# Kernel optimization log

Measured on AMD Instinct MI355X. Metric: run time of the kernel, lower is better.

Reference implementation:

```python
import math
import jax, jax.numpy as jnp
import numpy as np

E = 1024
H = 16
HD = E // H
MLP = 4 * E
EPS = 1e-6


def setup_inputs() -> dict:
    key = jax.random.key(0)
    ks = jax.random.split(key, 12)
    s = lambda fan_in: 1.0 / math.sqrt(fan_in)
    return {
        "x": jax.random.normal(ks[0], (8, 1024, E), dtype=jnp.float32),
        "ln1_g": jnp.ones((E,), jnp.float32),
        "ln1_b": jnp.zeros((E,), jnp.float32),
        "w_qkv": jax.random.normal(ks[1], (E, 3 * E), jnp.float32) * s(E),
        "b_qkv": jnp.zeros((3 * E,), jnp.float32),
        "w_o": jax.random.normal(ks[2], (E, E), jnp.float32) * s(E),
        "b_o": jnp.zeros((E,), jnp.float32),
        "ln2_g": jnp.ones((E,), jnp.float32),
        "ln2_b": jnp.zeros((E,), jnp.float32),
        "w_fc1": jax.random.normal(ks[3], (E, MLP), jnp.float32) * s(E),
        "b_fc1": jnp.zeros((MLP,), jnp.float32),
        "w_fc2": jax.random.normal(ks[4], (MLP, E), jnp.float32) * s(MLP),
        "b_fc2": jnp.zeros((E,), jnp.float32),
    }


def _layernorm(x, g, b):
    mu = jnp.mean(x, axis=-1, keepdims=True)
    var = jnp.mean(jnp.square(x - mu), axis=-1, keepdims=True)
    return (x - mu) * jax.lax.rsqrt(var + EPS) * g + b


def _attn(x, w_qkv, b_qkv, w_o, b_o):
    B, N, _ = x.shape
    qkv = (x @ w_qkv + b_qkv).reshape(B, N, 3, H, HD)
    q, k, v = qkv[:, :, 0], qkv[:, :, 1], qkv[:, :, 2]  # [B,N,H,HD]
    scores = jnp.einsum("bnhd,bmhd->bhnm", q, k) / math.sqrt(HD)
    probs = jax.nn.softmax(scores, axis=-1)
    out = jnp.einsum("bhnm,bmhd->bnhd", probs, v).reshape(B, N, H * HD)
    return out @ w_o + b_o


def reference(x, ln1_g, ln1_b, w_qkv, b_qkv, w_o, b_o, ln2_g, ln2_b,
              w_fc1, b_fc1, w_fc2, b_fc2):
    # pre-LN attention block with residual
    x = x + _attn(_layernorm(x, ln1_g, ln1_b), w_qkv, b_qkv, w_o, b_o)
    # pre-LN MLP block with residual (exact GELU, matching torch nn.GELU)
    h = _layernorm(x, ln2_g, ln2_b) @ w_fc1 + b_fc1
    h = jax.nn.gelu(h, approximate=False)
    x = x + (h @ w_fc2 + b_fc2)
    return x
```

## Files before the change

kernel.cpp:

```cpp
#include <hip/hip_runtime.h>
#include <stdint.h>

typedef unsigned short u16;
typedef __bf16 bf16x8 __attribute__((ext_vector_type(8)));
typedef float f32x4 __attribute__((ext_vector_type(4)));

#define GLD16(gp, lp) __builtin_amdgcn_global_load_lds( \
    (__attribute__((address_space(1))) void*)(uintptr_t)(gp), \
    (__attribute__((address_space(3))) void*)(uintptr_t)(lp), 16, 0, 0)

#define WAITVM(N) asm volatile("s_waitcnt vmcnt(" #N ")" ::: "memory")
#define BARRIER() asm volatile("s_barrier" ::: "memory")
#define MM(a, b, c) __builtin_amdgcn_mfma_f32_16x16x32_bf16(a, b, c, 0, 0, 0)

__device__ __forceinline__ u16 f2bf(float f) {
  uint32_t u = __builtin_bit_cast(uint32_t, f);
  u += 0x7FFFu + ((u >> 16) & 1u);
  return (u16)(u >> 16);
}

__global__ __launch_bounds__(256) void wtrans(const float* __restrict__ w,
                                              u16* __restrict__ wt, int K, int Nn) {
  __shared__ float tile[64][68];
  const int c0 = blockIdx.x << 6, r0 = blockIdx.y << 6;
  const int t = threadIdx.x, tr = t >> 2, tc = t & 3;
#pragma unroll
  for (int p = 0; p < 4; ++p) {
    float4 v = *(const float4*)&w[(size_t)(r0 + tr) * Nn + c0 + tc * 4 + p * 16];
    tile[tr][tc * 4 + p * 16 + 0] = v.x;
    tile[tr][tc * 4 + p * 16 + 1] = v.y;
    tile[tr][tc * 4 + p * 16 + 2] = v.z;
    tile[tr][tc * 4 + p * 16 + 3] = v.w;
  }
  __syncthreads();
#pragma unroll
  for (int p = 0; p < 4; ++p) {
    u16 e0 = f2bf(tile[tc * 4 + p * 16 + 0][tr]);
    u16 e1 = f2bf(tile[tc * 4 + p * 16 + 1][tr]);
    u16 e2 = f2bf(tile[tc * 4 + p * 16 + 2][tr]);
    u16 e3 = f2bf(tile[tc * 4 + p * 16 + 3][tr]);
    uint2 o;
    o.x = (uint32_t)e0 | ((uint32_t)e1 << 16);
    o.y = (uint32_t)e2 | ((uint32_t)e3 << 16);
    *(uint2*)&wt[(size_t)(c0 + tr) * K + r0 + tc * 4 + p * 16] = o;
  }
}

__global__ __launch_bounds__(256) void lnorm(const float* x, const float* __restrict__ g,
                                             const float* __restrict__ bta,
                                             u16* __restrict__ out) {
  const int lane = threadIdx.x & 63, wid = threadIdx.x >> 6;
  const size_t token = (size_t)blockIdx.x * 4 + wid;
  const float* row = x + token * 1024;
  float v[16];
#pragma unroll
  for (int i = 0; i < 4; ++i) {
    float4 f = *(const float4*)&row[(lane + i * 64) * 4];
    v[i * 4 + 0] = f.x; v[i * 4 + 1] = f.y; v[i * 4 + 2] = f.z; v[i * 4 + 3] = f.w;
  }
  float s = 0.f, s2 = 0.f;
#pragma unroll
  for (int i = 0; i < 16; ++i) { s += v[i]; s2 += v[i] * v[i]; }
  for (int off = 1; off < 64; off <<= 1) {
    s += __shfl_xor(s, off);
    s2 += __shfl_xor(s2, off);
  }
  const float mu = s * (1.0f / 1024.0f);
  const float var = s2 * (1.0f / 1024.0f) - mu * mu;
  const float rstd = rsqrtf(var + 1e-6f);
  u16* orow = out + token * 1024;
#pragma unroll
  for (int i = 0; i < 4; ++i) {
    const int c = (lane + i * 64) * 4;
    float4 gv = *(const float4*)&g[c];
    float4 bv = *(const float4*)&bta[c];
    u16 e0 = f2bf((v[i * 4 + 0] - mu) * rstd * gv.x + bv.x);
    u16 e1 = f2bf((v[i * 4 + 1] - mu) * rstd * gv.y + bv.y);
    u16 e2 = f2bf((v[i * 4 + 2] - mu) * rstd * gv.z + bv.z);
    u16 e3 = f2bf((v[i * 4 + 3] - mu) * rstd * gv.w + bv.w);
    uint2 o;
    o.x = (uint32_t)e0 | ((uint32_t)e1 << 16);
    o.y = (uint32_t)e2 | ((uint32_t)e3 << 16);
    *(uint2*)&orow[c] = o;
  }
}

template <int EPI>
__global__ __launch_bounds__(512, 2) void gemmk(const u16* __restrict__ A,
                                                const u16* __restrict__ Bt,
                                                const float* __restrict__ bias,
                                                void* Cout, int Ndim, int K, int nT,
                                                float qscale, int qlimit, int gn) {
  __shared__ __align__(16) u16 lds[4][16384];
  const int tid = threadIdx.x, lane = tid & 63, wid = tid >> 6;
  const int wm = wid >> 2, wn = wid & 3;

  const int wg = blockIdx.x;
  const int swz = (wg & 7) * ((int)gridDim.x >> 3) + (wg >> 3);
  const int mblk = swz / gn, nb = swz - mblk * gn;
  const int m0 = mblk << 8, n0 = nb << 8;
  const int koff = blockIdx.y * (nT << 5);

  const int srow = tid >> 2;
  const int gsub = (tid & 3) ^ ((tid >> 3) & 3);
  const u16* Ag = A + koff + (size_t)(m0 + srow) * K + gsub * 8;
  const u16* Bg = Bt + koff + (size_t)(n0 + srow) * K + gsub * 8;
  const size_t rstep = (size_t)128 * K;
  char* lb = (char*)&lds[0][0];

  const int rrow = lane & 15, g = lane >> 4;
  const int xg = g ^ ((rrow >> 1) & 3);
  const int aoff = (wm * 128 + rrow) * 64 + xg * 16;
  const int boff = 16384 + (wn * 64 + rrow) * 64 + xg * 16;

  const f32x4 fzero = {0.f, 0.f, 0.f, 0.f};
  f32x4 acc[8][4];
#pragma unroll
  for (int i = 0; i < 8; ++i)
#pragma unroll
    for (int j = 0; j < 4; ++j) acc[i][j] = fzero;

#define STG(tt) do { \
    char* d_ = lb + ((tt) & 3) * 32768; \
    GLD16(Ag + (size_t)(tt) * 32, d_ + tid * 16); \
    GLD16(Ag + rstep + (size_t)(tt) * 32, d_ + 8192 + tid * 16); \
    GLD16(Bg + (size_t)(tt) * 32, d_ + 16384 + tid * 16); \
    GLD16(Bg + rstep + (size_t)(tt) * 32, d_ + 24576 + tid * 16); \
  } while (0)

  STG(0);
  STG(1);
  WAITVM(4);
  BARRIER();
  for (int t = 0; t < nT; ++t) {
    if (t + 2 < nT) STG(t + 2);
    const char* sb = lb + (t & 3) * 32768;
    bf16x8 bfr[4], af[8];
#pragma unroll
    for (int nf = 0; nf < 4; ++nf)
      bfr[nf] = *(const bf16x8*)(sb + boff + nf * 1024);
#pragma unroll
    for (int mf = 0; mf < 8; ++mf)
      af[mf] = *(const bf16x8*)(sb + aoff + mf * 1024);
    __builtin_amdgcn_s_setprio(1);
#pragma unroll
    for (int mf = 0; mf < 8; ++mf)
#pragma unroll
      for (int nf = 0; nf < 4; ++nf)
        acc[mf][nf] = MM(af[mf], bfr[nf], acc[mf][nf]);
    __builtin_amdgcn_s_setprio(0);
    if (t + 1 < nT) {
      if (t < nT - 2) { WAITVM(4); } else { WAITVM(0); }
      BARRIER();
    }
  }
#undef STG

  const int g4 = (lane >> 4) << 2;
#pragma unroll
  for (int nf = 0; nf < 4; ++nf) {
    const int col = n0 + wn * 64 + nf * 16 + rrow;
    const float bvb = (EPI == 3 && blockIdx.y != 0) ? 0.0f : bias[col];
    const float csf = (EPI == 0 && col < qlimit) ? qscale : 1.0f;
#pragma unroll
    for (int mf = 0; mf < 8; ++mf) {
#pragma unroll
      for (int r = 0; r < 4; ++r) {
        const int row = m0 + wm * 128 + mf * 16 + g4 + r;
        float v = acc[mf][nf][r] + bvb;
        if (EPI == 0) v *= csf;
        if (EPI == 1) v = 0.5f * v * (1.0f + erff(v * 0.70710678118654752f));
        if (EPI == 3) {
          atomicAdd((float*)Cout + (size_t)row * Ndim + col, v);
        } else {
          ((u16*)Cout)[(size_t)row * Ndim + col] = f2bf(v);
        }
      }
    }
  }
}

__global__ __launch_bounds__(256) void vtrans(const u16* __restrict__ qkv,
                                              u16* __restrict__ vt) {
  const int bh = blockIdx.y, b = bh >> 4, h = bh & 15;
  const int n0 = blockIdx.x << 6;
  __shared__ __align__(16) u16 tile[64][72];
  const int t = threadIdx.x, r = t >> 2, c = t & 3;
  const u16* src = qkv + (size_t)((b << 10) + n0 + r) * 3072 + 2048 + (h << 6);
#pragma unroll
  for (int p = 0; p < 2; ++p)
    *(uint4*)&tile[r][(c * 2 + p) * 8] = *(const uint4*)(src + (c * 2 + p) * 8);
  __syncthreads();
  u16* dst = vt + (size_t)((bh << 6) + r) * 1024 + n0;
#pragma unroll
  for (int p = 0; p < 2; ++p) {
    u16 o[8];
#pragma unroll
    for (int j = 0; j < 8; ++j) o[j] = tile[(c * 2 + p) * 8 + j][r];
    uint4 w;
    w.x = (uint32_t)o[0] | ((uint32_t)o[1] << 16);
    w.y = (uint32_t)o[2] | ((uint32_t)o[3] << 16);
    w.z = (uint32_t)o[4] | ((uint32_t)o[5] << 16);
    w.w = (uint32_t)o[6] | ((uint32_t)o[7] << 16);
    *(uint4*)&dst[(c * 2 + p) * 8] = w;
  }
}

__global__ __launch_bounds__(256) void attn64(const u16* __restrict__ qkv,
                                              const u16* __restrict__ vt,
                                              u16* __restrict__ aout) {
  const int bh = blockIdx.y, b = bh >> 4, h = bh & 15;
  const int q0 = blockIdx.x << 6;
  const int tid = threadIdx.x, lane = tid & 63, wid = tid >> 6;
  __shared__ __align__(16) u16 kl[4096];
  __shared__ __align__(16) u16 vl[4096];
  __shared__ __align__(16) u16 pl[4][1152];

  const int rrow = lane & 15;
  const int g = lane >> 4;
  const u16* qrow = qkv + (size_t)((b << 10) + q0 + (wid << 4) + rrow) * 3072 + (h << 6);
  bf16x8 qf0 = *(const bf16x8*)(qrow + (g << 3));
  bf16x8 qf1 = *(const bf16x8*)(qrow + 32 + (g << 3));

  const int sr = lane >> 3;
  const int lc = (lane & 7) ^ sr;
  const u16* kbase = qkv + (size_t)(b << 10) * 3072 + 1024 + (h << 6) +
                     (size_t)(16 * wid + sr) * 3072 + lc * 8;
  const u16* vbase = vt + (size_t)(bh << 6) * 1024 + (size_t)(16 * wid + sr) * 1024 + lc * 8;

  const f32x4 fzero = {0.f, 0.f, 0.f, 0.f};
  f32x4 oacc[4];
#pragma unroll
  for (int i = 0; i < 4; ++i) oacc[i] = fzero;
  f32x4 lacc = fzero;
  const int rcb = lane & 7;
  u16* plw = &pl[wid][0];

  for (int t = 0; t < 16; ++t) {
    const int kt0 = t << 6;
    GLD16(kbase + (size_t)kt0 * 3072, &kl[(2 * wid + 0) * 512]);
    GLD16(kbase + (size_t)kt0 * 3072 + 8 * 3072, &kl[(2 * wid + 1) * 512]);
    GLD16(vbase + kt0, &vl[(2 * wid + 0) * 512]);
    GLD16(vbase + kt0 + 8 * 1024, &vl[(2 * wid + 1) * 512]);
    __syncthreads();

    f32x4 s4[4];
#pragma unroll
    for (int i = 0; i < 4; ++i) s4[i] = fzero;
#pragma unroll
    for (int nf = 0; nf < 4; ++nf) {
      bf16x8 k0 = *(const bf16x8*)((const char*)kl + (nf * 16 + rrow) * 128 +
                                   ((g + 0) ^ rcb) * 16);
      bf16x8 k1 = *(const bf16x8*)((const char*)kl + (nf * 16 + rrow) * 128 +
                                   ((g + 4) ^ rcb) * 16);
      s4[nf] = __builtin_amdgcn_mfma_f32_16x16x32_bf16(k0, qf0, s4[nf], 0, 0, 0);
      s4[nf] = __builtin_amdgcn_mfma_f32_16x16x32_bf16(k1, qf1, s4[nf], 0, 0, 0);
    }

#pragma unroll
    for (int nf = 0; nf < 4; ++nf) {
      float p0 = exp2f(s4[nf][0]);
      float p1 = exp2f(s4[nf][1]);
      float p2 = exp2f(s4[nf][2]);
      float p3 = exp2f(s4[nf][3]);
      f32x4 pv = {p0, p1, p2, p3};
      lacc += pv;
      uint32_t a0 = __builtin_bit_cast(uint32_t, p0) + 0x8000u;
      uint32_t a1 = __builtin_bit_cast(uint32_t, p1) + 0x8000u;
      uint32_t a2 = __builtin_bit_cast(uint32_t, p2) + 0x8000u;
      uint32_t a3 = __builtin_bit_cast(uint32_t, p3) + 0x8000u;
      uint2 w;
      w.x = __builtin_amdgcn_perm(a1, a0, 0x07060302);
      w.y = __builtin_amdgcn_perm(a3, a2, 0x07060302);
      *(uint2*)(plw + rrow * 72 + nf * 16 + (g << 2)) = w;
    }

    bf16x8 pf0 = *(const bf16x8*)((const char*)plw + rrow * 144 + (g << 4));
    bf16x8 pf1 = *(const bf16x8*)((const char*)plw + rrow * 144 + (g << 4) + 64);
#pragma unroll
    for (int nf = 0; nf < 4; ++nf) {
      bf16x8 v0 = *(const bf16x8*)((const char*)vl + (nf * 16 + rrow) * 128 +
                                   ((g + 0) ^ rcb) * 16);
      bf16x8 v1 = *(const bf16x8*)((const char*)vl + (nf * 16 + rrow) * 128 +
                                   ((g + 4) ^ rcb) * 16);
      oacc[nf] = __builtin_amdgcn_mfma_f32_16x16x32_bf16(pf0, v0, oacc[nf], 0, 0, 0);
      oacc[nf] = __builtin_amdgcn_mfma_f32_16x16x32_bf16(pf1, v1, oacc[nf], 0, 0, 0);
    }
    __syncthreads();
  }

  float lsum = lacc[0] + lacc[1] + lacc[2] + lacc[3];
  lsum += __shfl_xor(lsum, 16);
  lsum += __shfl_xor(lsum, 32);
  const float inv = 1.0f / lsum;
  float invq[4];
#pragma unroll
  for (int r = 0; r < 4; ++r) {
    int bi = __builtin_amdgcn_ds_bpermute(((g << 2) + r) << 2,
                                          __builtin_bit_cast(int, inv));
    invq[r] = __builtin_bit_cast(float, bi);
  }
  u16* ob = aout + (size_t)((b << 10) + q0 + (wid << 4)) * 1024 + (h << 6);
#pragma unroll
  for (int nf = 0; nf < 4; ++nf)
#pragma unroll
    for (int r = 0; r < 4; ++r)
      ob[(size_t)(g * 4 + r) * 1024 + nf * 16 + rrow] = f2bf(oacc[nf][r] * invq[r]);
}

extern "C" void kernel_launch(void* const* d_in, const int* in_sizes, int n_in,
                              void* d_out, int out_size, void* d_ws, size_t ws_size,
                              hipStream_t stream) {
  const float* x = (const float*)d_in[0];
  const float* ln1_g = (const float*)d_in[1];
  const float* ln1_b = (const float*)d_in[2];
  const float* w_qkv = (const float*)d_in[3];
  const float* b_qkv = (const float*)d_in[4];
  const float* w_o = (const float*)d_in[5];
  const float* b_o = (const float*)d_in[6];
  const float* ln2_g = (const float*)d_in[7];
  const float* ln2_b = (const float*)d_in[8];
  const float* w_fc1 = (const float*)d_in[9];
  const float* b_fc1 = (const float*)d_in[10];
  const float* w_fc2 = (const float*)d_in[11];
  const float* b_fc2 = (const float*)d_in[12];
  float* out = (float*)d_out;

  char* w = (char*)d_ws;
  u16* wqkvT = (u16*)w; w += (size_t)3072 * 1024 * 2;
  u16* woT   = (u16*)w; w += (size_t)1024 * 1024 * 2;
  u16* wfc1T = (u16*)w; w += (size_t)4096 * 1024 * 2;
  u16* wfc2T = (u16*)w; w += (size_t)1024 * 4096 * 2;
  u16* xn    = (u16*)w; w += (size_t)8192 * 1024 * 2;
  u16* qkvb  = (u16*)w; w += (size_t)8192 * 3072 * 2;
  u16* vtb   = (u16*)w; w += (size_t)128 * 64 * 1024 * 2;
  u16* attnb = (u16*)w; w += (size_t)8192 * 1024 * 2;
  u16* hbuf  = qkvb;

  const float QS = 0.18033688011112042f;

  wtrans<<<dim3(48, 16), 256, 0, stream>>>(w_qkv, wqkvT, 1024, 3072);
  wtrans<<<dim3(16, 16), 256, 0, stream>>>(w_o, woT, 1024, 1024);
  wtrans<<<dim3(64, 16), 256, 0, stream>>>(w_fc1, wfc1T, 1024, 4096);
  wtrans<<<dim3(16, 64), 256, 0, stream>>>(w_fc2, wfc2T, 4096, 1024);

  lnorm<<<2048, 256, 0, stream>>>(x, ln1_g, ln1_b, xn);
  gemmk<0><<<dim3(384, 1), 512, 0, stream>>>(xn, wqkvT, b_qkv, qkvb, 3072, 1024, 32, QS, 1024, 12);
  vtrans<<<dim3(16, 128), 256, 0, stream>>>(qkvb, vtb);
  attn64<<<dim3(16, 128), 256, 0, stream>>>(qkvb, vtb, attnb);
  hipMemcpyAsync(out, x, (size_t)8192 * 1024 * 4, hipMemcpyDeviceToDevice, stream);
  gemmk<3><<<dim3(128, 2), 512, 0, stream>>>(attnb, woT, b_o, out, 1024, 1024, 16, 1.f, 0, 4);
  lnorm<<<2048, 256, 0, stream>>>(out, ln2_g, ln2_b, xn);
  gemmk<1><<<dim3(512, 1), 512, 0, stream>>>(xn, wfc1T, b_fc1, hbuf, 4096, 1024, 32, 1.f, 0, 16);
  gemmk<3><<<dim3(128, 2), 512, 0, stream>>>(hbuf, wfc2T, b_fc2, out, 1024, 4096, 64, 1.f, 0, 4);
}
```

Baseline: 480.5 us.

## Deepen GEMM pipeline to three stages, split staging, replace split-K atomics with residual epilogue

```diff
diff --git a/kernel.cpp b/kernel.cpp
--- a/kernel.cpp
+++ b/kernel.cpp
@@ -86,11 +86,12 @@
 }
 
 template <int EPI>
-__global__ __launch_bounds__(512, 2) void gemmk(const u16* __restrict__ A,
+__global__ __launch_bounds__(512, 2) void gemmf(const u16* __restrict__ A,
                                                 const u16* __restrict__ Bt,
                                                 const float* __restrict__ bias,
-                                                void* Cout, int Ndim, int K, int nT,
-                                                float qscale, int qlimit, int gn) {
+                                                const float* res, void* Cout,
+                                                int Ndim, int K, float qscale,
+                                                int qlimit, int gn) {
   __shared__ __align__(16) u16 lds[4][16384];
   const int tid = threadIdx.x, lane = tid & 63, wid = tid >> 6;
   const int wm = wid >> 2, wn = wid & 3;
@@ -99,12 +100,11 @@
   const int swz = (wg & 7) * ((int)gridDim.x >> 3) + (wg >> 3);
   const int mblk = swz / gn, nb = swz - mblk * gn;
   const int m0 = mblk << 8, n0 = nb << 8;
-  const int koff = blockIdx.y * (nT << 5);
 
   const int srow = tid >> 2;
   const int gsub = (tid & 3) ^ ((tid >> 3) & 3);
-  const u16* Ag = A + koff + (size_t)(m0 + srow) * K + gsub * 8;
-  const u16* Bg = Bt + koff + (size_t)(n0 + srow) * K + gsub * 8;
+  const u16* Ag = A + (size_t)(m0 + srow) * K + gsub * 8;
+  const u16* Bg = Bt + (size_t)(n0 + srow) * K + gsub * 8;
   const size_t rstep = (size_t)128 * K;
   char* lb = (char*)&lds[0][0];
 
@@ -120,47 +120,69 @@
 #pragma unroll
     for (int j = 0; j < 4; ++j) acc[i][j] = fzero;
 
-#define STG(tt) do { \
-    char* d_ = lb + ((tt) & 3) * 32768; \
+#define STGA(tt) do { char* d_ = lb + ((tt) & 3) * 32768; \
     GLD16(Ag + (size_t)(tt) * 32, d_ + tid * 16); \
-    GLD16(Ag + rstep + (size_t)(tt) * 32, d_ + 8192 + tid * 16); \
+    GLD16(Ag + rstep + (size_t)(tt) * 32, d_ + 8192 + tid * 16); } while (0)
+#define STGB(tt) do { char* d_ = lb + ((tt) & 3) * 32768; \
     GLD16(Bg + (size_t)(tt) * 32, d_ + 16384 + tid * 16); \
-    GLD16(Bg + rstep + (size_t)(tt) * 32, d_ + 24576 + tid * 16); \
-  } while (0)
-
-  STG(0);
-  STG(1);
-  WAITVM(4);
-  BARRIER();
-  for (int t = 0; t < nT; ++t) {
-    if (t + 2 < nT) STG(t + 2);
-    const char* sb = lb + (t & 3) * 32768;
-    bf16x8 bfr[4], af[8];
-#pragma unroll
-    for (int nf = 0; nf < 4; ++nf)
-      bfr[nf] = *(const bf16x8*)(sb + boff + nf * 1024);
-#pragma unroll
-    for (int mf = 0; mf < 8; ++mf)
-      af[mf] = *(const bf16x8*)(sb + aoff + mf * 1024);
+    GLD16(Bg + rstep + (size_t)(tt) * 32, d_ + 24576 + tid * 16); } while (0)
+
+  const int nT = K >> 5;
+  STGA(0); STGB(0);
+  STGA(1); STGB(1);
+  STGA(2); STGB(2);
+
+  for (int k = 0; k < nT; ++k) {
+    if (k < nT - 2) { WAITVM(8); }
+    else if (k == nT - 2) { WAITVM(4); }
+    else { WAITVM(0); }
+    BARRIER();
+    const char* sb = lb + (k & 3) * 32768;
+    const bool st = (k + 3 < nT);
+    if (st) STGA(k + 3);
+    bf16x8 a0 = *(const bf16x8*)(sb + aoff + 0 * 1024);
+    bf16x8 a1 = *(const bf16x8*)(sb + aoff + 1 * 1024);
+    bf16x8 a2 = *(const bf16x8*)(sb + aoff + 2 * 1024);
+    bf16x8 a3 = *(const bf16x8*)(sb + aoff + 3 * 1024);
+    bf16x8 a4 = *(const bf16x8*)(sb + aoff + 4 * 1024);
+    bf16x8 a5 = *(const bf16x8*)(sb + aoff + 5 * 1024);
+    bf16x8 a6 = *(const bf16x8*)(sb + aoff + 6 * 1024);
+    bf16x8 a7 = *(const bf16x8*)(sb + aoff + 7 * 1024);
+    bf16x8 b0 = *(const bf16x8*)(sb + boff + 0 * 1024);
+    bf16x8 b1 = *(const bf16x8*)(sb + boff + 1 * 1024);
     __builtin_amdgcn_s_setprio(1);
-#pragma unroll
-    for (int mf = 0; mf < 8; ++mf)
-#pragma unroll
-      for (int nf = 0; nf < 4; ++nf)
-        acc[mf][nf] = MM(af[mf], bfr[nf], acc[mf][nf]);
+    acc[0][0] = MM(a0, b0, acc[0][0]); acc[1][0] = MM(a1, b0, acc[1][0]);
+    acc[2][0] = MM(a2, b0, acc[2][0]); acc[3][0] = MM(a3, b0, acc[3][0]);
+    acc[4][0] = MM(a4, b0, acc[4][0]); acc[5][0] = MM(a5, b0, acc[5][0]);
+    acc[6][0] = MM(a6, b0, acc[6][0]); acc[7][0] = MM(a7, b0, acc[7][0]);
+    acc[0][1] = MM(a0, b1, acc[0][1]); acc[1][1] = MM(a1, b1, acc[1][1]);
+    acc[2][1] = MM(a2, b1, acc[2][1]); acc[3][1] = MM(a3, b1, acc[3][1]);
+    acc[4][1] = MM(a4, b1, acc[4][1]); acc[5][1] = MM(a5, b1, acc[5][1]);
+    acc[6][1] = MM(a6, b1, acc[6][1]); acc[7][1] = MM(a7, b1, acc[7][1]);
     __builtin_amdgcn_s_setprio(0);
-    if (t + 1 < nT) {
-      if (t < nT - 2) { WAITVM(4); } else { WAITVM(0); }
-      BARRIER();
-    }
-  }
-#undef STG
+    BARRIER();
+    if (st) STGB(k + 3);
+    bf16x8 b2 = *(const bf16x8*)(sb + boff + 2 * 1024);
+    bf16x8 b3 = *(const bf16x8*)(sb + boff + 3 * 1024);
+    __builtin_amdgcn_s_setprio(1);
+    acc[0][2] = MM(a0, b2, acc[0][2]); acc[1][2] = MM(a1, b2, acc[1][2]);
+    acc[2][2] = MM(a2, b2, acc[2][2]); acc[3][2] = MM(a3, b2, acc[3][2]);
+    acc[4][2] = MM(a4, b2, acc[4][2]); acc[5][2] = MM(a5, b2, acc[5][2]);
+    acc[6][2] = MM(a6, b2, acc[6][2]); acc[7][2] = MM(a7, b2, acc[7][2]);
+    acc[0][3] = MM(a0, b3, acc[0][3]); acc[1][3] = MM(a1, b3, acc[1][3]);
+    acc[2][3] = MM(a2, b3, acc[2][3]); acc[3][3] = MM(a3, b3, acc[3][3]);
+    acc[4][3] = MM(a4, b3, acc[4][3]); acc[5][3] = MM(a5, b3, acc[5][3]);
+    acc[6][3] = MM(a6, b3, acc[6][3]); acc[7][3] = MM(a7, b3, acc[7][3]);
+    __builtin_amdgcn_s_setprio(0);
+  }
+#undef STGA
+#undef STGB
 
   const int g4 = (lane >> 4) << 2;
 #pragma unroll
   for (int nf = 0; nf < 4; ++nf) {
     const int col = n0 + wn * 64 + nf * 16 + rrow;
-    const float bvb = (EPI == 3 && blockIdx.y != 0) ? 0.0f : bias[col];
+    const float bvb = bias[col];
     const float csf = (EPI == 0 && col < qlimit) ? qscale : 1.0f;
 #pragma unroll
     for (int mf = 0; mf < 8; ++mf) {
@@ -170,8 +192,9 @@
         float v = acc[mf][nf][r] + bvb;
         if (EPI == 0) v *= csf;
         if (EPI == 1) v = 0.5f * v * (1.0f + erff(v * 0.70710678118654752f));
-        if (EPI == 3) {
-          atomicAdd((float*)Cout + (size_t)row * Ndim + col, v);
+        if (EPI == 2) {
+          v += res[(size_t)row * Ndim + col];
+          ((float*)Cout)[(size_t)row * Ndim + col] = v;
         } else {
           ((u16*)Cout)[(size_t)row * Ndim + col] = f2bf(v);
         }
@@ -345,12 +368,11 @@
   wtrans<<<dim3(16, 64), 256, 0, stream>>>(w_fc2, wfc2T, 4096, 1024);
 
   lnorm<<<2048, 256, 0, stream>>>(x, ln1_g, ln1_b, xn);
-  gemmk<0><<<dim3(384, 1), 512, 0, stream>>>(xn, wqkvT, b_qkv, qkvb, 3072, 1024, 32, QS, 1024, 12);
+  gemmf<0><<<384, 512, 0, stream>>>(xn, wqkvT, b_qkv, nullptr, qkvb, 3072, 1024, QS, 1024, 12);
   vtrans<<<dim3(16, 128), 256, 0, stream>>>(qkvb, vtb);
   attn64<<<dim3(16, 128), 256, 0, stream>>>(qkvb, vtb, attnb);
-  hipMemcpyAsync(out, x, (size_t)8192 * 1024 * 4, hipMemcpyDeviceToDevice, stream);
-  gemmk<3><<<dim3(128, 2), 512, 0, stream>>>(attnb, woT, b_o, out, 1024, 1024, 16, 1.f, 0, 4);
+  gemmf<2><<<128, 512, 0, stream>>>(attnb, woT, b_o, x, out, 1024, 1024, 1.f, 0, 4);
   lnorm<<<2048, 256, 0, stream>>>(out, ln2_g, ln2_b, xn);
-  gemmk<1><<<dim3(512, 1), 512, 0, stream>>>(xn, wfc1T, b_fc1, hbuf, 4096, 1024, 32, 1.f, 0, 16);
-  gemmk<3><<<dim3(128, 2), 512, 0, stream>>>(hbuf, wfc2T, b_fc2, out, 1024, 4096, 64, 1.f, 0, 4);
-}
+  gemmf<1><<<512, 512, 0, stream>>>(xn, wfc1T, b_fc1, nullptr, hbuf, 4096, 1024, 1.f, 0, 16);
+  gemmf<2><<<128, 512, 0, stream>>>(hbuf, wfc2T, b_fc2, out, out, 1024, 4096, 1.f, 0, 4);
+}
```

Result: no change. 477.2 us (-0.7%).
